# Kernel optimization log

Hardware: AMD Instinct MI355X
Metric: run time of the kernel (lower is better)

Reference implementation:

```python
import jax, jax.numpy as jnp
import numpy as np

H, W = 480, 640          # sensor resolution (self.dim)
N = 16_777_216           # number of events


def setup_inputs() -> dict:
    key = jax.random.key(0)
    k1, k2, k3, k4 = jax.random.split(key, 4)
    x = jax.random.randint(k1, (N,), 0, W).astype(jnp.float32)
    y = jax.random.randint(k2, (N,), 0, H).astype(jnp.float32)
    t = jax.random.uniform(k3, (N,), minval=1e-3, maxval=1.0)
    p = jax.random.randint(k4, (N,), 0, 2).astype(jnp.float32) * 2.0 - 1.0  # {-1, +1}
    events = jnp.stack([x, y, t, p], axis=1)  # [N, 4]
    return {"events": events}


def reference(events):
    # events: [N, 4] columns (x, y, t, p)
    x, y, t, p = events.T
    t = t / t.max()          # computed in original (unused for indexing)
    p = (p + 1.0) / 2.0      # {-1,1} -> {0,1}
    idx = (x + W * y + W * H * p).astype(jnp.int32)  # [N] flat voxel index
    # scatter-add event counts, then binarize (vox_ec[vox_ec > 0] = 1)
    vox = jnp.zeros(2 * H * W, dtype=events.dtype).at[idx].add(jnp.ones_like(x))
    vox = jnp.where(vox > 0, jnp.ones_like(vox), vox)
    return vox.reshape(-1, 2, H, W)  # [1, 2, H, W]
```

## Files before the change

### kernel.cpp

```cpp
#include <hip/hip_runtime.h>
#include <hip/hip_bf16.h>

#define EW 640
#define EH 480
#define NVOX (2 * EH * EW)
#define NWORDS (NVOX / 32)
#define BLK 512
#define NBLOCKS 512
#define NCHUNK 8

typedef float vf4 __attribute__((ext_vector_type(4)));

__device__ __forceinline__ int ev_idx(vf4 e) {
    float p01 = (e.w + 1.0f) * 0.5f;
    return (int)(e.x + (float)EW * e.y + (float)(EW * EH) * p01);
}

__global__ void __launch_bounds__(BLK, 4)
event_bitmap_kernel(const vf4* __restrict__ events,
                    unsigned int* __restrict__ bms, int n) {
    __shared__ unsigned int bm[NWORDS];
    for (int w = threadIdx.x; w < NWORDS; w += BLK) bm[w] = 0u;
    __syncthreads();

    const int nth = gridDim.x * BLK;
    int i = blockIdx.x * BLK + threadIdx.x;
    for (; i + 3 * nth < n; i += 4 * nth) {
        vf4 e0 = events[i];
        vf4 e1 = events[i + nth];
        vf4 e2 = events[i + 2 * nth];
        vf4 e3 = events[i + 3 * nth];
        int x0 = ev_idx(e0), x1 = ev_idx(e1), x2 = ev_idx(e2), x3 = ev_idx(e3);
        atomicOr(&bm[x0 >> 5], 1u << (x0 & 31));
        atomicOr(&bm[x1 >> 5], 1u << (x1 & 31));
        atomicOr(&bm[x2 >> 5], 1u << (x2 & 31));
        atomicOr(&bm[x3 >> 5], 1u << (x3 & 31));
    }
    for (; i < n; i += nth) {
        vf4 e = events[i];
        int x = ev_idx(e);
        atomicOr(&bm[x >> 5], 1u << (x & 31));
    }
    __syncthreads();

    uint4* dst = (uint4*)(bms + (size_t)blockIdx.x * NWORDS);
    const uint4* src = (const uint4*)bm;
    for (int w = threadIdx.x; w < NWORDS / 4; w += BLK) dst[w] = src[w];
}

__global__ void __launch_bounds__(256)
reduce_kernel(const unsigned int* __restrict__ bms,
              unsigned int* __restrict__ partial) {
    int w = blockIdx.x * 256 + threadIdx.x;
    int b0 = blockIdx.y * (NBLOCKS / NCHUNK);
    unsigned int acc = 0u;
    #pragma unroll 8
    for (int b = 0; b < NBLOCKS / NCHUNK; ++b)
        acc |= bms[(size_t)(b0 + b) * NWORDS + w];
    partial[(size_t)blockIdx.y * NWORDS + w] = acc;
}

__global__ void __launch_bounds__(256)
expand_kernel(const unsigned int* __restrict__ partial,
              float* __restrict__ out) {
    int w = blockIdx.x * 256 + threadIdx.x;
    unsigned int acc = 0u;
    #pragma unroll
    for (int c = 0; c < NCHUNK; ++c)
        acc |= partial[(size_t)c * NWORDS + w];
    vf4* dst = (vf4*)(out + (size_t)w * 32);
    #pragma unroll
    for (int q = 0; q < 8; ++q) {
        vf4 v;
        v.x = (acc >> (q * 4 + 0)) & 1u ? 1.0f : 0.0f;
        v.y = (acc >> (q * 4 + 1)) & 1u ? 1.0f : 0.0f;
        v.z = (acc >> (q * 4 + 2)) & 1u ? 1.0f : 0.0f;
        v.w = (acc >> (q * 4 + 3)) & 1u ? 1.0f : 0.0f;
        dst[q] = v;
    }
}

extern "C" void kernel_launch(void* const* d_in, const int* in_sizes, int n_in,
                              void* d_out, int out_size, void* d_ws, size_t ws_size,
                              hipStream_t stream) {
    const vf4* events = (const vf4*)d_in[0];
    float* out = (float*)d_out;
    int n = in_sizes[0] / 4;

    unsigned int* bms = (unsigned int*)d_ws;
    unsigned int* partial = bms + (size_t)NBLOCKS * NWORDS;

    event_bitmap_kernel<<<NBLOCKS, BLK, 0, stream>>>(events, bms, n);
    reduce_kernel<<<dim3(NWORDS / 256, NCHUNK), 256, 0, stream>>>(bms, partial);
    expand_kernel<<<NWORDS / 256, 256, 0, stream>>>(partial, out);
}
```

Before: 369.3 us.

## Halve bitmap blocks, unroll event loads, coalesce expand stores via shared memory

The event pass now uses 256 blocks of 1024 threads instead of 512 of 512 and issues 8 independent event loads per iteration. This halves the number of per-block bitmaps written to and re-read from the workspace. The reduce stage is retuned to 16 chunks to match. The expand kernel stages each block's words in shared memory so consecutive threads write consecutive float4s, replacing the old 128-byte-strided per-thread stores. The costs are larger blocks with possible occupancy limits, extra register pressure, and an added barrier in expand.

```diff
diff --git a/kernel.cpp b/kernel.cpp
--- a/kernel.cpp
+++ b/kernel.cpp
@@ -5,9 +5,9 @@
 #define EH 480
 #define NVOX (2 * EH * EW)
 #define NWORDS (NVOX / 32)
-#define BLK 512
-#define NBLOCKS 512
-#define NCHUNK 8
+#define BLKA 1024
+#define NBLK_A 256
+#define NCHUNK 16
 
 typedef float vf4 __attribute__((ext_vector_type(4)));
 
@@ -16,25 +16,34 @@
     return (int)(e.x + (float)EW * e.y + (float)(EW * EH) * p01);
 }
 
-__global__ void __launch_bounds__(BLK, 4)
+__global__ void __launch_bounds__(BLKA, 4)
 event_bitmap_kernel(const vf4* __restrict__ events,
                     unsigned int* __restrict__ bms, int n) {
     __shared__ unsigned int bm[NWORDS];
-    for (int w = threadIdx.x; w < NWORDS; w += BLK) bm[w] = 0u;
+    for (int w = threadIdx.x; w < NWORDS; w += BLKA) bm[w] = 0u;
     __syncthreads();
 
-    const int nth = gridDim.x * BLK;
-    int i = blockIdx.x * BLK + threadIdx.x;
-    for (; i + 3 * nth < n; i += 4 * nth) {
+    const int nth = gridDim.x * BLKA;
+    int i = blockIdx.x * BLKA + threadIdx.x;
+    for (; i + 7 * nth < n; i += 8 * nth) {
         vf4 e0 = events[i];
         vf4 e1 = events[i + nth];
         vf4 e2 = events[i + 2 * nth];
         vf4 e3 = events[i + 3 * nth];
+        vf4 e4 = events[i + 4 * nth];
+        vf4 e5 = events[i + 5 * nth];
+        vf4 e6 = events[i + 6 * nth];
+        vf4 e7 = events[i + 7 * nth];
         int x0 = ev_idx(e0), x1 = ev_idx(e1), x2 = ev_idx(e2), x3 = ev_idx(e3);
+        int x4 = ev_idx(e4), x5 = ev_idx(e5), x6 = ev_idx(e6), x7 = ev_idx(e7);
         atomicOr(&bm[x0 >> 5], 1u << (x0 & 31));
         atomicOr(&bm[x1 >> 5], 1u << (x1 & 31));
         atomicOr(&bm[x2 >> 5], 1u << (x2 & 31));
         atomicOr(&bm[x3 >> 5], 1u << (x3 & 31));
+        atomicOr(&bm[x4 >> 5], 1u << (x4 & 31));
+        atomicOr(&bm[x5 >> 5], 1u << (x5 & 31));
+        atomicOr(&bm[x6 >> 5], 1u << (x6 & 31));
+        atomicOr(&bm[x7 >> 5], 1u << (x7 & 31));
     }
     for (; i < n; i += nth) {
         vf4 e = events[i];
@@ -45,17 +54,17 @@
 
     uint4* dst = (uint4*)(bms + (size_t)blockIdx.x * NWORDS);
     const uint4* src = (const uint4*)bm;
-    for (int w = threadIdx.x; w < NWORDS / 4; w += BLK) dst[w] = src[w];
+    for (int w = threadIdx.x; w < NWORDS / 4; w += BLKA) dst[w] = src[w];
 }
 
 __global__ void __launch_bounds__(256)
 reduce_kernel(const unsigned int* __restrict__ bms,
               unsigned int* __restrict__ partial) {
     int w = blockIdx.x * 256 + threadIdx.x;
-    int b0 = blockIdx.y * (NBLOCKS / NCHUNK);
+    int b0 = blockIdx.y * (NBLK_A / NCHUNK);
     unsigned int acc = 0u;
-    #pragma unroll 8
-    for (int b = 0; b < NBLOCKS / NCHUNK; ++b)
+    #pragma unroll
+    for (int b = 0; b < NBLK_A / NCHUNK; ++b)
         acc |= bms[(size_t)(b0 + b) * NWORDS + w];
     partial[(size_t)blockIdx.y * NWORDS + w] = acc;
 }
@@ -63,20 +72,27 @@
 __global__ void __launch_bounds__(256)
 expand_kernel(const unsigned int* __restrict__ partial,
               float* __restrict__ out) {
+    __shared__ unsigned int sbm[256];
     int w = blockIdx.x * 256 + threadIdx.x;
     unsigned int acc = 0u;
     #pragma unroll
     for (int c = 0; c < NCHUNK; ++c)
         acc |= partial[(size_t)c * NWORDS + w];
-    vf4* dst = (vf4*)(out + (size_t)w * 32);
+    sbm[threadIdx.x] = acc;
+    __syncthreads();
+
+    vf4* out4 = (vf4*)out + (size_t)blockIdx.x * 2048;
     #pragma unroll
     for (int q = 0; q < 8; ++q) {
+        int f = q * 256 + threadIdx.x;
+        unsigned int wv = sbm[f >> 3];
+        int sh = (f & 7) * 4;
         vf4 v;
-        v.x = (acc >> (q * 4 + 0)) & 1u ? 1.0f : 0.0f;
-        v.y = (acc >> (q * 4 + 1)) & 1u ? 1.0f : 0.0f;
-        v.z = (acc >> (q * 4 + 2)) & 1u ? 1.0f : 0.0f;
-        v.w = (acc >> (q * 4 + 3)) & 1u ? 1.0f : 0.0f;
-        dst[q] = v;
+        v.x = (wv >> (sh + 0)) & 1u ? 1.0f : 0.0f;
+        v.y = (wv >> (sh + 1)) & 1u ? 1.0f : 0.0f;
+        v.z = (wv >> (sh + 2)) & 1u ? 1.0f : 0.0f;
+        v.w = (wv >> (sh + 3)) & 1u ? 1.0f : 0.0f;
+        out4[f] = v;
     }
 }
 
@@ -88,9 +104,9 @@
     int n = in_sizes[0] / 4;
 
     unsigned int* bms = (unsigned int*)d_ws;
-    unsigned int* partial = bms + (size_t)NBLOCKS * NWORDS;
+    unsigned int* partial = bms + (size_t)NBLK_A * NWORDS;
 
-    event_bitmap_kernel<<<NBLOCKS, BLK, 0, stream>>>(events, bms, n);
+    event_bitmap_kernel<<<NBLK_A, BLKA, 0, stream>>>(events, bms, n);
     reduce_kernel<<<dim3(NWORDS / 256, NCHUNK), 256, 0, stream>>>(bms, partial);
     expand_kernel<<<NWORDS / 256, 256, 0, stream>>>(partial, out);
 }
```

After: 364.3 us. No clear change (-1.4%).
